# Kernel tuning notes

Measured on AMD Instinct MI355X. Metric: run time of the kernel, lower is better.

The kernel has to match this reference:

```python
import jax, jax.numpy as jnp
import numpy as np
import math

D_MODEL = 1024
NUM_HEADS = 16
D_HEAD = D_MODEL // NUM_HEADS
BATCH = 2
SEQ = 2048
ROPE_BASE = 10000.0


def get_rotary_embedding(seq_len, d_head):
    # standard RoPE tables: cos/sin of shape [seq_len, d_head]
    inv_freq = 1.0 / (ROPE_BASE ** (jnp.arange(0, d_head, 2, dtype=jnp.float32) / d_head))
    t = jnp.arange(seq_len, dtype=jnp.float32)
    freqs = jnp.outer(t, inv_freq)                      # [S, d_head/2]
    emb = jnp.concatenate([freqs, freqs], axis=-1)      # [S, d_head]
    return jnp.cos(emb), jnp.sin(emb)


def rotate_half(x):
    x1, x2 = jnp.split(x, 2, axis=-1)
    return jnp.concatenate([-x2, x1], axis=-1)


def apply_rotary_pos_emb(x, cos, sin):
    # x: [B, H, S, Dh]; cos/sin: [S, Dh] broadcast over B, H
    return x * cos[None, None, :, :] + rotate_half(x) * sin[None, None, :, :]


def setup_inputs() -> dict:
    key = jax.random.key(0)
    ks = jax.random.split(key, 9)
    s = 1.0 / math.sqrt(D_MODEL)
    inp = {
        "x":  jax.random.normal(ks[0], (BATCH, SEQ, D_MODEL), dtype=jnp.float32),
        "Wq": jax.random.uniform(ks[1], (D_MODEL, D_MODEL), jnp.float32, -s, s),
        "bq": jnp.zeros((D_MODEL,), jnp.float32),
        "Wk": jax.random.uniform(ks[2], (D_MODEL, D_MODEL), jnp.float32, -s, s),
        "bk": jnp.zeros((D_MODEL,), jnp.float32),
        "Wv": jax.random.uniform(ks[3], (D_MODEL, D_MODEL), jnp.float32, -s, s),
        "bv": jnp.zeros((D_MODEL,), jnp.float32),
        "Wo": jax.random.uniform(ks[4], (D_MODEL, D_MODEL), jnp.float32, -s, s),
        "bo": jnp.zeros((D_MODEL,), jnp.float32),
    }
    return inp


def reference(x, Wq, bq, Wk, bk, Wv, bv, Wo, bo) -> jnp.ndarray:
    B, S, _ = x.shape
    H, Dh = NUM_HEADS, D_HEAD

    def proj(W, b):
        y = jnp.einsum('bsd,ed->bse', x, W) + b          # nn.Linear: x @ W^T + b
        return y.reshape(B, S, H, Dh).transpose(0, 2, 1, 3)  # [B,H,S,Dh]

    Q = proj(Wq, bq)
    K = proj(Wk, bk)
    V = proj(Wv, bv)

    cos, sin = get_rotary_embedding(S, Dh)
    Q = apply_rotary_pos_emb(Q, cos, sin)
    K = apply_rotary_pos_emb(K, cos, sin)

    scores = jnp.einsum('bhqd,bhkd->bhqk', Q, K) / math.sqrt(Dh)  # [B,H,S,S]
    causal = jnp.tril(jnp.ones((S, S), dtype=bool))
    scores = jnp.where(causal[None, None, :, :], scores, -jnp.inf)
    attn = jax.nn.softmax(scores, axis=-1)
    # dropout is identity in eval / p=0
    context = jnp.einsum('bhqk,bhkd->bhqd', attn, V)               # [B,H,S,Dh]
    context = context.transpose(0, 2, 1, 3).reshape(B, S, H * Dh)
    return jnp.einsum('bsd,ed->bse', context, Wo) + bo
```

## Files before the change

### kernel.cpp

```cpp
#include <hip/hip_runtime.h>
#include <hip/hip_bf16.h>
#include <math.h>

typedef __attribute__((ext_vector_type(8))) short short8;
typedef __attribute__((ext_vector_type(8))) __bf16 bf16x8;
typedef __attribute__((ext_vector_type(4))) float f32x4;
typedef __attribute__((ext_vector_type(16))) float f32x16;

#define D_MODEL 1024
#define NUM_HEADS 16
#define D_HEAD 64
#define BATCH 2
#define SEQ 2048
#define BH (BATCH * NUM_HEADS)
#define MTOT (BATCH * SEQ)

__device__ inline f32x4 mfma16(short8 a, short8 b, f32x4 c) {
  return __builtin_amdgcn_mfma_f32_16x16x32_bf16(
      __builtin_bit_cast(bf16x8, a), __builtin_bit_cast(bf16x8, b), c, 0, 0, 0);
}

__device__ inline f32x16 mfma32(short8 a, short8 b, f32x16 c) {
  return __builtin_amdgcn_mfma_f32_32x32x16_bf16(
      __builtin_bit_cast(bf16x8, a), __builtin_bit_cast(bf16x8, b), c, 0, 0, 0);
}

__device__ inline unsigned short f2b(float f) {
  __hip_bfloat16 h = __float2bfloat16(f);
  return __builtin_bit_cast(unsigned short, h);
}

__device__ inline unsigned cvt_pk_bf16(float lo, float hi) {
  unsigned r;
  asm("v_cvt_pk_bf16_f32 %0, %1, %2" : "=v"(r) : "v"(lo), "v"(hi));
  return r;
}

__device__ inline float exp2_hw(float x) {
  float r;
  asm("v_exp_f32 %0, %1" : "=v"(r) : "v"(x));
  return r;
}

__device__ inline void permlane32_swap(unsigned& a, unsigned& b) {
  asm("v_permlane32_swap_b32 %0, %1" : "+v"(a), "+v"(b));
}

__device__ __forceinline__ void wait_barrier_vm0() {
  asm volatile("s_waitcnt vmcnt(0)\n\ts_barrier" ::: "memory");
}

#define GLOAD_LDS16(gaddr, laddr)                                              \
  __builtin_amdgcn_global_load_lds(                                            \
      (const __attribute__((address_space(1))) void*)(gaddr),                  \
      (__attribute__((address_space(3))) void*)(laddr), 16, 0, 0)

__global__ void prep(const float* __restrict__ x,
                     const float* __restrict__ Wq, const float* __restrict__ Wk,
                     const float* __restrict__ Wv, const float* __restrict__ Wo,
                     unsigned short* __restrict__ xb,
                     unsigned short* __restrict__ wqkv,
                     unsigned short* __restrict__ wob,
                     float2* __restrict__ tct) {
  const int bid = blockIdx.x;
  if (bid < 8192) {
    const float* in;
    unsigned short* out;
    int lb;
    if (bid < 4096) {
      in = x; out = xb; lb = bid;
    } else {
      const int q = (bid - 4096) >> 10;
      lb = (bid - 4096) & 1023;
      in = (q == 0) ? Wq : (q == 1) ? Wk : (q == 2) ? Wv : Wo;
      out = (q < 3) ? wqkv + (size_t)q * 1048576 : wob;
    }
    int i = (lb * 256 + threadIdx.x) * 4;
    float4 v = *(const float4*)(in + i);
    ushort4 o;
    o.x = f2b(v.x); o.y = f2b(v.y); o.z = f2b(v.z); o.w = f2b(v.w);
    *(ushort4*)(out + i) = o;
  } else {
    int idx = (bid - 8192) * 256 + threadIdx.x;
    int i = idx & 31;
    int s = idx >> 5;
    float inv = powf(10000.0f, -(float)i / 32.0f);
    float t = (float)s * inv;
    tct[idx] = make_float2(cosf(t), sinf(t));
  }
}

#define STAGE64(t, bufi)                                                        \
  do {                                                                          \
    const int _k0 = (t) * 64;                                                   \
    const int _gc = ((lane & 7) ^ (lane >> 3)) * 8;                             \
    const int _lc = (lane & 7) * 8;                                             \
    for (int j = 0; j < 4; j++) {                                               \
      const int _r = w * 32 + j * 8 + (lane >> 3);                              \
      GLOAD_LDS16(&A[(size_t)(bm + _r) * D_MODEL + _k0 + _gc], &As[bufi][_r][_lc]); \
      GLOAD_LDS16(&Bp[(size_t)(bn + _r) * D_MODEL + _k0 + _gc], &Bs[bufi][_r][_lc]); \
    }                                                                           \
  } while (0)

#define KLOOP64()                                                               \
  do {                                                                          \
    const int NT = D_MODEL / 64;                                                \
    STAGE64(0, 0);                                                              \
    for (int t = 0; t < NT; ++t) {                                              \
      const int cur = t & 1;                                                    \
      wait_barrier_vm0();                                                       \
      if (t + 1 < NT) STAGE64(t + 1, cur ^ 1);                                  \
      for (int kk = 0; kk < 2; kk++) {                                          \
        short8 af[4], bf4[4];                                                   \
        for (int mi = 0; mi < 4; mi++)                                          \
          af[mi] = *(const short8*)&As[cur][wr + mi * 16 + fr]                  \
                                         [(kk * 32 + fk) ^ ((fr & 7) << 3)];    \
        for (int ni = 0; ni < 4; ni++)                                          \
          bf4[ni] = *(const short8*)&Bs[cur][wc + ni * 16 + fr]                 \
                                          [(kk * 32 + fk) ^ ((fr & 7) << 3)];   \
        __builtin_amdgcn_s_setprio(1);                                          \
        for (int mi = 0; mi < 4; mi++)                                          \
          for (int ni = 0; ni < 4; ni++)                                        \
            acc[mi][ni] = mfma16(af[mi], bf4[ni], acc[mi][ni]);                 \
        __builtin_amdgcn_s_setprio(0);                                          \
      }                                                                         \
    }                                                                           \
  } while (0)

__global__ __launch_bounds__(256) void gemm_qkv(
    const unsigned short* __restrict__ A,
    const unsigned short* __restrict__ Bp,
    const float* __restrict__ bq, const float* __restrict__ bk,
    const float* __restrict__ bv,
    const float2* __restrict__ tct,
    unsigned short* __restrict__ Qb, unsigned short* __restrict__ Kb,
    unsigned short* __restrict__ Vt) {
  __shared__ unsigned short As[2][128][64];
  __shared__ unsigned short Bs[2][128][64];
  const int bm = blockIdx.y * 128;
  const int bn = blockIdx.x * 128;
  const int tid = threadIdx.x;
  const int lane = tid & 63;
  const int w = tid >> 6;
  const int wr = (w >> 1) * 64, wc = (w & 1) * 64;
  const int fr = lane & 15;
  const int g = lane >> 4;
  const int fk = g * 8;

  f32x4 acc[4][4] = {};
  KLOOP64();

  const int type = bn >> 10;
  const int cloc = (bn & 1023) + wc;
  if (type <= 1) {
    const float* bias = (type == 0) ? bq : bk;
    unsigned short* outp = (type == 0) ? Qb : Kb;
    const float SC = (type == 0) ? 0.125f * 1.44269504f : 1.0f;
    const int h = cloc >> 6;
    for (int mi = 0; mi < 4; mi++)
      for (int r = 0; r < 4; r++) {
        int row = bm + wr + mi * 16 + g * 4 + r;
        int b = row >> 11, s = row & (SEQ - 1);
        size_t base = (((size_t)(b * NUM_HEADS + h)) * SEQ + s) * 64;
        for (int ni = 0; ni < 2; ni++) {
          int i = ni * 16 + fr;
          float x0 = acc[mi][ni][r] + bias[cloc + i];
          float x1 = acc[mi][ni + 2][r] + bias[cloc + i + 32];
          float2 cs = tct[s * 32 + i];
          outp[base + i]      = f2b((x0 * cs.x - x1 * cs.y) * SC);
          outp[base + i + 32] = f2b((x1 * cs.x + x0 * cs.y) * SC);
        }
      }
  } else {
    for (int mi = 0; mi < 4; mi++) {
      int row0 = bm + wr + mi * 16 + g * 4;
      int b = row0 >> 11, s0 = row0 & (SEQ - 1);
      for (int ni = 0; ni < 4; ni++) {
        int col = cloc + ni * 16 + fr;
        int h = col >> 6, dh = col & 63;
        float bvv = bv[col];
        uint2 pk = make_uint2(
            cvt_pk_bf16(acc[mi][ni][0] + bvv, acc[mi][ni][1] + bvv),
            cvt_pk_bf16(acc[mi][ni][2] + bvv, acc[mi][ni][3] + bvv));
        *(uint2*)&Vt[(((size_t)(b * NUM_HEADS + h)) * 64 + dh) * SEQ + s0] = pk;
      }
    }
  }
}

__global__ __launch_bounds__(256) void gemm_out(
    const unsigned short* __restrict__ A,
    const unsigned short* __restrict__ Bp,
    const float* __restrict__ bias,
    float* __restrict__ outf) {
  __shared__ unsigned short As[2][128][64];
  __shared__ unsigned short Bs[2][128][64];
  const int bm = blockIdx.y * 128;
  const int bn = blockIdx.x * 128;
  const int tid = threadIdx.x;
  const int lane = tid & 63;
  const int w = tid >> 6;
  const int wr = (w >> 1) * 64, wc = (w & 1) * 64;
  const int fr = lane & 15;
  const int g = lane >> 4;
  const int fk = g * 8;

  f32x4 acc[4][4] = {};
  KLOOP64();

  for (int mi = 0; mi < 4; mi++)
    for (int ni = 0; ni < 4; ni++)
      for (int r = 0; r < 4; r++) {
        int row = bm + wr + mi * 16 + g * 4 + r;
        int col = bn + wc + ni * 16 + fr;
        outf[(size_t)row * D_MODEL + col] = acc[mi][ni][r] + bias[col];
      }
}

__global__ __launch_bounds__(512) void flash_attn(
    const unsigned short* __restrict__ Q,
    const unsigned short* __restrict__ Km,
    const unsigned short* __restrict__ Vt,
    unsigned short* __restrict__ ctx) {
  __shared__ unsigned short Ks[2][64 * 64];
  __shared__ unsigned short Vs[2][64 * 64];
  const int bh = blockIdx.x;
  const int by = blockIdx.y;
  const int tid = threadIdx.x;
  const int lane = tid & 63;
  const int w = tid >> 6;
  const int gi = w >> 2;
  const int wl = w & 3;
  const int q31 = lane & 31;
  const int hi = lane >> 5;

  const unsigned short* Qp = Q + (size_t)bh * SEQ * 64;
  const unsigned short* Kp = Km + (size_t)bh * SEQ * 64;
  const unsigned short* Vp = Vt + (size_t)bh * 64 * SEQ;
  const int b = bh >> 4, h = bh & 15;

  const int qt = gi ? by : (15 - by);
  const int qbase = qt * 128;
  const int qrow0 = qbase + wl * 32;
  const int wmax = qrow0 + 31;
  const int q = qrow0 + q31;

  short8 qf[4];
  for (int s = 0; s < 4; s++)
    qf[s] = *(const short8*)&Qp[(size_t)q * 64 + s * 16 + hi * 8];

  const int srow = tid >> 3;
  const int ss = tid & 7;
  const int lw = srow * 64 + ((ss ^ (srow & 7)) * 8);

  short8 kr = *(const short8*)&Kp[(size_t)srow * 64 + ss * 8];
  short8 vr = *(const short8*)&Vp[(size_t)srow * SEQ + ss * 8];

  f32x16 oacc0 = {}, oacc1 = {};
  float lq = 0.f;
  const int NSTEPS = 2 * (15 - by) + 2;

  for (int step = 0; step < NSTEPS; ++step) {
    const int kbase = step * 64;
    const int cur = step & 1;
    *(short8*)&Ks[cur][lw] = kr;
    *(short8*)&Vs[cur][lw] = vr;
    __syncthreads();
    if (step + 1 < NSTEPS) {
      const int nk = kbase + 64;
      kr = *(const short8*)&Kp[(size_t)(nk + srow) * 64 + ss * 8];
      vr = *(const short8*)&Vp[(size_t)srow * SEQ + nk + ss * 8];
    }

    if (kbase <= wmax) {
      for (int kt = 0; kt < 2; kt++) {
        const int ktb = kbase + kt * 32;
        if (ktb <= wmax) {
          f32x16 sacc = {};
          const int krow = kt * 32 + q31;
          const int kro = krow * 64;
          const int ksw = krow & 7;
          for (int s = 0; s < 4; s++) {
            short8 kf = *(const short8*)&Ks[cur][kro + (((s * 2 + hi) ^ ksw) * 8)];
            sacc = mfma32(kf, qf[s], sacc);
          }
          const bool maskT = (ktb + 31 > qrow0);
          float p[16];
          float rs = 0.f;
#pragma unroll
          for (int reg = 0; reg < 16; reg++) {
            float sv = sacc[reg];
            if (maskT) {
              int key = ktb + (reg & 3) + 8 * (reg >> 2) + 4 * hi;
              sv = (key <= q) ? sv : -INFINITY;
            }
            p[reg] = exp2_hw(sv);
            rs += p[reg];
          }
          lq += rs;
          short8 paf[2];
#pragma unroll
          for (int sl = 0; sl < 2; sl++) {
            const int o = sl * 8;
            unsigned a0 = cvt_pk_bf16(p[o + 0], p[o + 1]);
            unsigned b0 = cvt_pk_bf16(p[o + 4], p[o + 5]);
            permlane32_swap(a0, b0);
            unsigned a1 = cvt_pk_bf16(p[o + 2], p[o + 3]);
            unsigned b1 = cvt_pk_bf16(p[o + 6], p[o + 7]);
            permlane32_swap(a1, b1);
            uint4 u = make_uint4(a0, a1, b0, b1);
            paf[sl] = __builtin_bit_cast(short8, u);
          }
#pragma unroll
          for (int dt = 0; dt < 2; dt++) {
            const int vrow = dt * 32 + q31;
            const int vro = vrow * 64;
            const int vsw = vrow & 7;
#pragma unroll
            for (int sl = 0; sl < 2; sl++) {
              short8 vf = *(const short8*)&Vs[cur][vro + (((kt * 4 + sl * 2 + hi) ^ vsw) * 8)];
              if (dt == 0) oacc0 = mfma32(paf[sl], vf, oacc0);
              else         oacc1 = mfma32(paf[sl], vf, oacc1);
            }
          }
        }
      }
    }
  }

  lq += __shfl_xor(lq, 32);
#pragma unroll
  for (int reg = 0; reg < 16; reg++) {
    const int crow = (reg & 3) + 8 * (reg >> 2) + 4 * hi;
    const float linv = 1.f / __shfl(lq, crow);
    const int row = qrow0 + crow;
    size_t base = ((size_t)b * SEQ + row) * D_MODEL + h * 64 + q31;
    ctx[base]      = f2b(oacc0[reg] * linv);
    ctx[base + 32] = f2b(oacc1[reg] * linv);
  }
}

extern "C" void kernel_launch(void* const* d_in, const int* in_sizes, int n_in,
                              void* d_out, int out_size, void* d_ws, size_t ws_size,
                              hipStream_t stream) {
  const float* x  = (const float*)d_in[0];
  const float* Wq = (const float*)d_in[1];
  const float* bq = (const float*)d_in[2];
  const float* Wk = (const float*)d_in[3];
  const float* bk = (const float*)d_in[4];
  const float* Wv = (const float*)d_in[5];
  const float* bv = (const float*)d_in[6];
  const float* Wo = (const float*)d_in[7];
  const float* bo = (const float*)d_in[8];
  float* out = (float*)d_out;

  char* ws = (char*)d_ws;
  size_t off = 0;
  auto alloc = [&](size_t bytes) {
    char* p = ws + off;
    off += (bytes + 255) & ~(size_t)255;
    return p;
  };
  unsigned short* xb   = (unsigned short*)alloc((size_t)MTOT * D_MODEL * 2);
  unsigned short* wqkv = (unsigned short*)alloc((size_t)3 * D_MODEL * D_MODEL * 2);
  unsigned short* wob  = (unsigned short*)alloc((size_t)D_MODEL * D_MODEL * 2);
  unsigned short* Qb   = (unsigned short*)alloc((size_t)BH * SEQ * 64 * 2);
  unsigned short* Kb   = (unsigned short*)alloc((size_t)BH * SEQ * 64 * 2);
  unsigned short* Vt   = (unsigned short*)alloc((size_t)BH * 64 * SEQ * 2);
  unsigned short* ctxb = (unsigned short*)alloc((size_t)MTOT * D_MODEL * 2);
  float2* tct = (float2*)alloc((size_t)SEQ * 32 * 8);

  prep<<<8448, 256, 0, stream>>>(x, Wq, Wk, Wv, Wo, xb, wqkv, wob, tct);

  gemm_qkv<<<dim3(3 * D_MODEL / 128, MTOT / 128), 256, 0, stream>>>(
      xb, wqkv, bq, bk, bv, tct, Qb, Kb, Vt);

  flash_attn<<<dim3(BH, 8), 512, 0, stream>>>(Qb, Kb, Vt, ctxb);

  gemm_out<<<dim3(D_MODEL / 128, MTOT / 128), 256, 0, stream>>>(ctxb, wob, bo, out);
}
```

Baseline: 116.1 us.

## Process both paired causal query tiles per wave in 256-thread attention blocks

Each attention block now uses 4 waves instead of 8, and every wave computes two 32-row query slices: one from the high query tile and one from the low tile. Both reuse the same K/V LDS tile per step. Each thread loads two K and two V chunks per step to fill the shared tiles. This halves the waves contending for each LDS tile and interleaves two independent MFMA chains per wave. In exchange, register pressure roughly doubles and there are fewer waves per block.

Result: slower. 124.3 us (+7.0%).

```diff
diff --git a/kernel.cpp b/kernel.cpp
--- a/kernel.cpp
+++ b/kernel.cpp
@@ -217,7 +217,63 @@
       }
 }
 
-__global__ __launch_bounds__(512) void flash_attn(
+#define FTILE(qrow0_, q_, qf_, o0_, o1_, lq_)                                  \
+  if (kbase <= qrow0_ + 31) {                                                  \
+    for (int kt = 0; kt < 2; kt++) {                                           \
+      const int ktb = kbase + kt * 32;                                         \
+      if (ktb <= qrow0_ + 31) {                              \
+        f32x16 sacc = {};                                                      \
+        const int krow = kt * 32 + q31;                                        \
+        const int kro = krow * 64;                                             \
+        const int ksw = krow & 7;                                              \
+        for (int s = 0; s < 4; s++) {                                          \
+          short8 kf = *(const short8*)&Ks[cur][kro + (((s * 2 + hi) ^ ksw) * 8)]; \
+          sacc = mfma32(kf, qf_[s], sacc);                                     \
+        }                                                                      \
+        const bool maskT = (ktb + 31 > qrow0_);                                \
+        float p[16];                                                           \
+        float rs = 0.f;                                                        \
+        _Pragma("unroll")                                                      \
+        for (int reg = 0; reg < 16; reg++) {                                   \
+          float sv = sacc[reg];                                                \
+          if (maskT) {                                                         \
+            int key = ktb + (reg & 3) + 8 * (reg >> 2) + 4 * hi;               \
+            sv = (key <= q_) ? sv : -INFINITY;                                 \
+          }                                                                    \
+          p[reg] = exp2_hw(sv);                                                \
+          rs += p[reg];                                                        \
+        }                                                                      \
+        lq_ += rs;                                                             \
+        short8 paf[2];                                                         \
+        _Pragma("unroll")                                                      \
+        for (int sl = 0; sl < 2; sl++) {                                       \
+          const int o = sl * 8;                                                \
+          unsigned a0 = cvt_pk_bf16(p[o + 0], p[o + 1]);                       \
+          unsigned b0 = cvt_pk_bf16(p[o + 4], p[o + 5]);                       \
+          permlane32_swap(a0, b0);                                             \
+          unsigned a1 = cvt_pk_bf16(p[o + 2], p[o + 3]);                       \
+          unsigned b1 = cvt_pk_bf16(p[o + 6], p[o + 7]);                       \
+          permlane32_swap(a1, b1);                                             \
+          uint4 u = make_uint4(a0, a1, b0, b1);                                \
+          paf[sl] = __builtin_bit_cast(short8, u);                             \
+        }                                                                      \
+        _Pragma("unroll")                                                      \
+        for (int dt = 0; dt < 2; dt++) {                                       \
+          const int vrow = dt * 32 + q31;                                      \
+          const int vro = vrow * 64;                                           \
+          const int vsw = vrow & 7;                                            \
+          _Pragma("unroll")                                                    \
+          for (int sl = 0; sl < 2; sl++) {                                     \
+            short8 vf = *(const short8*)&Vs[cur][vro + (((kt * 4 + sl * 2 + hi) ^ vsw) * 8)]; \
+            if (dt == 0) o0_ = mfma32(paf[sl], vf, o0_);                       \
+            else         o1_ = mfma32(paf[sl], vf, o1_);                       \
+          }                                                                    \
+        }                                                                      \
+      }                                                                        \
+    }                                                                          \
+  }
+
+__global__ __launch_bounds__(256) void flash_attn(
     const unsigned short* __restrict__ Q,
     const unsigned short* __restrict__ Km,
     const unsigned short* __restrict__ Vt,
@@ -229,8 +285,6 @@
   const int tid = threadIdx.x;
   const int lane = tid & 63;
   const int w = tid >> 6;
-  const int gi = w >> 2;
-  const int wl = w & 3;
   const int q31 = lane & 31;
   const int hi = lane >> 5;
 
@@ -239,104 +293,68 @@
   const unsigned short* Vp = Vt + (size_t)bh * 64 * SEQ;
   const int b = bh >> 4, h = bh & 15;
 
-  const int qt = gi ? by : (15 - by);
-  const int qbase = qt * 128;
-  const int qrow0 = qbase + wl * 32;
-  const int wmax = qrow0 + 31;
-  const int q = qrow0 + q31;
-
-  short8 qf[4];
-  for (int s = 0; s < 4; s++)
-    qf[s] = *(const short8*)&Qp[(size_t)q * 64 + s * 16 + hi * 8];
-
-  const int srow = tid >> 3;
-  const int ss = tid & 7;
-  const int lw = srow * 64 + ((ss ^ (srow & 7)) * 8);
-
-  short8 kr = *(const short8*)&Kp[(size_t)srow * 64 + ss * 8];
-  short8 vr = *(const short8*)&Vp[(size_t)srow * SEQ + ss * 8];
-
-  f32x16 oacc0 = {}, oacc1 = {};
-  float lq = 0.f;
-  const int NSTEPS = 2 * (15 - by) + 2;
+  const int qtH = 15 - by, qtL = by;
+  const int qrow0H = qtH * 128 + w * 32;
+  const int qrow0L = qtL * 128 + w * 32;
+  const int qH = qrow0H + q31;
+  const int qL = qrow0L + q31;
+
+  short8 qfH[4], qfL[4];
+#pragma unroll
+  for (int s = 0; s < 4; s++) {
+    qfH[s] = *(const short8*)&Qp[(size_t)qH * 64 + s * 16 + hi * 8];
+    qfL[s] = *(const short8*)&Qp[(size_t)qL * 64 + s * 16 + hi * 8];
+  }
+
+  const int srow = tid >> 2;
+  const int ss0 = (tid & 3) * 2, ss1 = ss0 + 1;
+  const int lw0 = srow * 64 + ((ss0 ^ (srow & 7)) * 8);
+  const int lw1 = srow * 64 + ((ss1 ^ (srow & 7)) * 8);
+
+  short8 krA = *(const short8*)&Kp[(size_t)srow * 64 + ss0 * 8];
+  short8 krB = *(const short8*)&Kp[(size_t)srow * 64 + ss1 * 8];
+  short8 vrA = *(const short8*)&Vp[(size_t)srow * SEQ + ss0 * 8];
+  short8 vrB = *(const short8*)&Vp[(size_t)srow * SEQ + ss1 * 8];
+
+  f32x16 oH0 = {}, oH1 = {}, oL0 = {}, oL1 = {};
+  float lqH = 0.f, lqL = 0.f;
+  const int NSTEPS = 2 * qtH + 2;
 
   for (int step = 0; step < NSTEPS; ++step) {
     const int kbase = step * 64;
     const int cur = step & 1;
-    *(short8*)&Ks[cur][lw] = kr;
-    *(short8*)&Vs[cur][lw] = vr;
+    *(short8*)&Ks[cur][lw0] = krA;
+    *(short8*)&Ks[cur][lw1] = krB;
+    *(short8*)&Vs[cur][lw0] = vrA;
+    *(short8*)&Vs[cur][lw1] = vrB;
     __syncthreads();
     if (step + 1 < NSTEPS) {
       const int nk = kbase + 64;
-      kr = *(const short8*)&Kp[(size_t)(nk + srow) * 64 + ss * 8];
-      vr = *(const short8*)&Vp[(size_t)srow * SEQ + nk + ss * 8];
+      krA = *(const short8*)&Kp[(size_t)(nk + srow) * 64 + ss0 * 8];
+      krB = *(const short8*)&Kp[(size_t)(nk + srow) * 64 + ss1 * 8];
+      vrA = *(const short8*)&Vp[(size_t)srow * SEQ + nk + ss0 * 8];
+      vrB = *(const short8*)&Vp[(size_t)srow * SEQ + nk + ss1 * 8];
     }
 
-    if (kbase <= wmax) {
-      for (int kt = 0; kt < 2; kt++) {
-        const int ktb = kbase + kt * 32;
-        if (ktb <= wmax) {
-          f32x16 sacc = {};
-          const int krow = kt * 32 + q31;
-          const int kro = krow * 64;
-          const int ksw = krow & 7;
-          for (int s = 0; s < 4; s++) {
-            short8 kf = *(const short8*)&Ks[cur][kro + (((s * 2 + hi) ^ ksw) * 8)];
-            sacc = mfma32(kf, qf[s], sacc);
-          }
-          const bool maskT = (ktb + 31 > qrow0);
-          float p[16];
-          float rs = 0.f;
-#pragma unroll
-          for (int reg = 0; reg < 16; reg++) {
-            float sv = sacc[reg];
-            if (maskT) {
-              int key = ktb + (reg & 3) + 8 * (reg >> 2) + 4 * hi;
-              sv = (key <= q) ? sv : -INFINITY;
-            }
-            p[reg] = exp2_hw(sv);
-            rs += p[reg];
-          }
-          lq += rs;
-          short8 paf[2];
-#pragma unroll
-          for (int sl = 0; sl < 2; sl++) {
-            const int o = sl * 8;
-            unsigned a0 = cvt_pk_bf16(p[o + 0], p[o + 1]);
-            unsigned b0 = cvt_pk_bf16(p[o + 4], p[o + 5]);
-            permlane32_swap(a0, b0);
-            unsigned a1 = cvt_pk_bf16(p[o + 2], p[o + 3]);
-            unsigned b1 = cvt_pk_bf16(p[o + 6], p[o + 7]);
-            permlane32_swap(a1, b1);
-            uint4 u = make_uint4(a0, a1, b0, b1);
-            paf[sl] = __builtin_bit_cast(short8, u);
-          }
-#pragma unroll
-          for (int dt = 0; dt < 2; dt++) {
-            const int vrow = dt * 32 + q31;
-            const int vro = vrow * 64;
-            const int vsw = vrow & 7;
-#pragma unroll
-            for (int sl = 0; sl < 2; sl++) {
-              short8 vf = *(const short8*)&Vs[cur][vro + (((kt * 4 + sl * 2 + hi) ^ vsw) * 8)];
-              if (dt == 0) oacc0 = mfma32(paf[sl], vf, oacc0);
-              else         oacc1 = mfma32(paf[sl], vf, oacc1);
-            }
-          }
-        }
-      }
-    }
-  }
-
-  lq += __shfl_xor(lq, 32);
+    FTILE(qrow0H, qH, qfH, oH0, oH1, lqH);
+    FTILE(qrow0L, qL, qfL, oL0, oL1, lqL);
+  }
+
+  lqH += __shfl_xor(lqH, 32);
+  lqL += __shfl_xor(lqL, 32);
 #pragma unroll
   for (int reg = 0; reg < 16; reg++) {
     const int crow = (reg & 3) + 8 * (reg >> 2) + 4 * hi;
-    const float linv = 1.f / __shfl(lq, crow);
-    const int row = qrow0 + crow;
-    size_t base = ((size_t)b * SEQ + row) * D_MODEL + h * 64 + q31;
-    ctx[base]      = f2b(oacc0[reg] * linv);
-    ctx[base + 32] = f2b(oacc1[reg] * linv);
+    const float linvH = 1.f / __shfl(lqH, crow);
+    const float linvL = 1.f / __shfl(lqL, crow);
+    const int rowH = qrow0H + crow;
+    const int rowL = qrow0L + crow;
+    size_t baseH = ((size_t)b * SEQ + rowH) * D_MODEL + h * 64 + q31;
+    size_t baseL = ((size_t)b * SEQ + rowL) * D_MODEL + h * 64 + q31;
+    ctx[baseH]      = f2b(oH0[reg] * linvH);
+    ctx[baseH + 32] = f2b(oH1[reg] * linvH);
+    ctx[baseL]      = f2b(oL0[reg] * linvL);
+    ctx[baseL + 32] = f2b(oL1[reg] * linvL);
   }
 }
 
@@ -375,7 +393,7 @@
   gemm_qkv<<<dim3(3 * D_MODEL / 128, MTOT / 128), 256, 0, stream>>>(
       xb, wqkv, bq, bk, bv, tct, Qb, Kb, Vt);
 
-  flash_attn<<<dim3(BH, 8), 512, 0, stream>>>(Qb, Kb, Vt, ctxb);
+  flash_attn<<<dim3(BH, 8), 256, 0, stream>>>(Qb, Kb, Vt, ctxb);
 
   gemm_out<<<dim3(D_MODEL / 128, MTOT / 128), 256, 0, stream>>>(ctxb, wob, bo, out);
 }
```
